# Kernel optimization log

Hardware: AMD Instinct MI355X
Metric: run time of the kernel (lower is better)

The kernel has to match this reference:

```python
import jax, jax.numpy as jnp
import numpy as np
from jax import lax

D_MAX = 6.4; GRID_RES = 0.1; G = 9.81; MASS = 40.0
K_STIFF = 5000.0; K_DAMP = float(np.sqrt(4.0 * MASS * K_STIFF)); K_FRIC = 0.5
DT = 0.01; N_STEPS = 500; EPS = 1e-6


def _robot_geometry():
    # DPhysConfig.rigid_body_geometry(from_mesh=False), robot_size=(1.0, 0.5)
    xs = np.concatenate([np.linspace(-0.5, 0.5, 8), np.linspace(-0.5, 0.5, 8)])
    ys = np.concatenate([0.25 * np.ones(8), -0.25 * np.ones(8)])
    zz = np.array([0.2, 0.1, 0.0, 0.0, 0.0, 0.0, 0.1, 0.2])
    zs = np.concatenate([zz, zz])
    pts = np.stack([xs, ys, zs], 1).astype(np.float32)
    cog = pts.mean(0)
    return pts, (pts[:, 1] > cog[1]), (pts[:, 1] < cog[1])


def _inertia_inv(mass, pts):
    n = pts.shape[0]; mp = mass / n
    x, y, z = pts[:, 0], pts[:, 1], pts[:, 2]
    Ixx = (mp * (y**2 + z**2)).sum(); Iyy = (mp * (x**2 + z**2)).sum(); Izz = (mp * (x**2 + y**2)).sum()
    Ixy = -(mp * x * y).sum(); Ixz = -(mp * x * z).sum(); Iyz = -(mp * y * z).sum()
    I = np.array([[Ixx, Ixy, Ixz], [Ixy, Iyy, Iyz], [Ixz, Iyz, Izz]], dtype=np.float64) * 10.0
    return np.linalg.inv(I).astype(np.float32)


def _interp(grid, xq, yq):
    # bilinear interpolation of (B,H,W) grid at metric query points (B,N)
    B, H, W = grid.shape
    xi = jnp.clip((xq + D_MAX) / GRID_RES, 0.0, H - 2)
    yi = jnp.clip((yq + D_MAX) / GRID_RES, 0.0, W - 2)
    x0 = jnp.floor(xi).astype(jnp.int32); y0 = jnp.floor(yi).astype(jnp.int32)
    b = jnp.arange(B)[:, None]
    z00 = grid[b, x0, y0];     z10 = grid[b, x0 + 1, y0]
    z01 = grid[b, x0, y0 + 1]; z11 = grid[b, x0 + 1, y0 + 1]
    wx = xi - x0; wy = yi - y0
    return z00 * (1 - wx) * (1 - wy) + z10 * wx * (1 - wy) + z01 * (1 - wx) * wy + z11 * wx * wy


def _normals(grid, xq, yq):
    e = GRID_RES
    dzdx = (_interp(grid, xq + e, yq) - _interp(grid, xq - e, yq)) / (2 * e)
    dzdy = (_interp(grid, xq, yq + e) - _interp(grid, xq, yq - e)) / (2 * e)
    n = jnp.stack([-dzdx, -dzdy, jnp.ones_like(dzdx)], -1)
    return n / (jnp.linalg.norm(n, axis=-1, keepdims=True) + EPS)


def _skew(v):
    z = jnp.zeros_like(v[..., 0])
    return jnp.stack([
        jnp.stack([z, -v[..., 2], v[..., 1]], -1),
        jnp.stack([v[..., 2], z, -v[..., 0]], -1),
        jnp.stack([-v[..., 1], v[..., 0], z], -1)], -2)


def _rk4(x, xd, dt):
    k1 = dt * xd
    k2 = dt * (xd + k1 / 2)
    k3 = dt * (xd + k2 / 2)
    k4 = dt * (xd + k3)
    return x + (k1 + 2 * k2 + 2 * k3 + k4) / 6


def _integrate_rotation(R, omega, dt):
    Ox = _skew(omega)                                  # (B,3,3)
    theta = jnp.linalg.norm(omega, axis=-1)[:, None, None]
    Oxn = Ox / (theta + EPS)
    I3 = jnp.eye(3, dtype=R.dtype)
    return R @ (I3 + Oxn * jnp.sin(theta * dt) + (Oxn @ Oxn) * (1 - jnp.cos(theta * dt)))


def _forward_sim(z_grid, controls, robot_points, I_inv, mask_left, mask_right):
    B = z_grid.shape[0]; n_pts = robot_points.shape[0]
    dt = jnp.float32(DT)
    x = jnp.zeros((B, 3), z_grid.dtype).at[:, 2].set(1.0)
    xd = jnp.zeros((B, 3), z_grid.dtype)
    R = jnp.broadcast_to(jnp.eye(3, dtype=z_grid.dtype), (B, 3, 3))
    omega = jnp.zeros((B, 3), z_grid.dtype)
    x_points = x[:, None, :] + robot_points[None]      # (B,n,3)
    xd_points = jnp.zeros((B, n_pts, 3), z_grid.dtype)
    ml = mask_left[None, :, None]; mr = mask_right[None, :, None]

    def step(carry, u):
        x, xd, R, omega, x_points, xd_points = carry
        u_left, u_right = u[:, 0], u[:, 1]
        # --- forward_kinematics ---
        z_pts = _interp(z_grid, x_points[..., 0], x_points[..., 1])[..., None]
        dh = x_points[..., 2:3] - z_pts
        on_grid = ((x_points[..., 0:1] >= -D_MAX) & (x_points[..., 0:1] <= D_MAX) &
                   (x_points[..., 1:2] >= -D_MAX) & (x_points[..., 1:2] <= D_MAX))
        in_contact = ((dh <= 0.0) & on_grid).astype(x_points.dtype)
        n = _normals(z_grid, x_points[..., 0], x_points[..., 1])   # (B,n,3)
        xd_n = (xd_points * n).sum(-1, keepdims=True)
        F_spring = -(K_STIFF * dh + K_DAMP * xd_n) * n * in_contact
        thrust = R[..., 0]                                         # R @ [1,0,0]
        thrust = thrust / (jnp.linalg.norm(thrust, axis=-1, keepdims=True) + EPS)
        N = jnp.linalg.norm(F_spring, axis=2)[..., None]           # (B,n,1)
        v_l = (u_left[:, None] * thrust)[:, None, :]
        v_r = (u_right[:, None] * thrust)[:, None, :]
        f_l = K_FRIC * N * jnp.tanh(v_l - xd_points)
        f_r = K_FRIC * N * jnp.tanh(v_r - xd_points)
        F_fric = jnp.where(ml, f_l, jnp.where(mr, f_r, jnp.zeros_like(f_l)))
        r = x_points - x[:, None, :]
        torque = jnp.cross(r, F_spring + F_fric).sum(1)            # (B,3)
        omega_d = torque @ I_inv.T
        F_cog = jnp.array([0.0, 0.0, -MASS * G], z_grid.dtype) + F_spring.mean(1) + F_fric.mean(1)
        xdd = F_cog / MASS
        xd_pts_new = xd[:, None, :] + jnp.cross(omega[:, None, :], r)
        # --- update_state ---
        xd_new = _rk4(xd, xdd, dt)
        x_new = _rk4(x, xd_new, dt)
        x_points_new = _rk4(x_points, xd_pts_new, dt)
        omega_new = _rk4(omega, omega_d, dt)
        R_new = _integrate_rotation(R, omega_new, dt)
        carry_new = (x_new, xd_new, R_new, omega_new, x_points_new, xd_pts_new)
        out = jnp.concatenate([x_new, xd_new, omega_new, R_new.reshape(B, 9),
                               x_points_new.reshape(B, -1),
                               F_spring.reshape(B, -1), F_fric.reshape(B, -1)], -1)
        return carry_new, out

    _, traj = lax.scan(step, (x, xd, R, omega, x_points, xd_points),
                       jnp.swapaxes(controls, 0, 1))
    return jnp.swapaxes(traj, 0, 1)   # (B, T, 3+3+3+9+48+48+48=162)


def setup_inputs() -> dict:
    key = jax.random.key(0)
    k1, k2 = jax.random.split(key)
    B, H, W, T = 256, 128, 128, N_STEPS
    pts, ml, mr = _robot_geometry()
    z_grid = 0.1 * jax.random.normal(k1, (B, H, W), dtype=jnp.float32)
    controls = jax.random.uniform(k2, (B, T, 2), dtype=jnp.float32, minval=-1.2, maxval=1.2)
    return {
        "z_grid": z_grid,
        "controls": controls,
        "robot_points": jnp.asarray(pts),
        "I_inv": jnp.asarray(_inertia_inv(MASS, pts)),
        "mask_left": jnp.asarray(ml),
        "mask_right": jnp.asarray(mr),
    }


def reference(z_grid, controls, robot_points, I_inv, mask_left, mask_right):
    return _forward_sim(z_grid, controls, robot_points, I_inv, mask_left, mask_right)
```

## Files before the change

### kernel.cpp

```cpp
#include <hip/hip_runtime.h>
#include <math.h>

#define HGRID 128
#define WGRID 128
#define NPTS 16
#define TSTEPS 500

__device__ __forceinline__ float dpp_sum16(float v) {
    int x;
    x = __builtin_amdgcn_update_dpp(0, __float_as_int(v), 0xB1, 0xF, 0xF, true);
    v += __int_as_float(x);
    x = __builtin_amdgcn_update_dpp(0, __float_as_int(v), 0x4E, 0xF, 0xF, true);
    v += __int_as_float(x);
    x = __builtin_amdgcn_update_dpp(0, __float_as_int(v), 0x141, 0xF, 0xF, true);
    v += __int_as_float(x);
    x = __builtin_amdgcn_update_dpp(0, __float_as_int(v), 0x140, 0xF, 0xF, true);
    v += __int_as_float(x);
    return v;
}

__device__ __forceinline__ float interp1(const float* __restrict__ sg, float xq, float yq) {
    float xi = (xq + 6.4f) / 0.1f;
    xi = fminf(fmaxf(xi, 0.0f), 126.0f);
    float yi = (yq + 6.4f) / 0.1f;
    yi = fminf(fmaxf(yi, 0.0f), 126.0f);
    float fx = floorf(xi);
    float fy = floorf(yi);
    int x0 = (int)fx;
    int y0 = (int)fy;
    float wx = xi - fx;
    float wy = yi - fy;
    const float* r0 = sg + (x0 * WGRID + y0);
    float z00 = r0[0];
    float z01 = r0[1];
    float z10 = r0[WGRID];
    float z11 = r0[WGRID + 1];
    float ox = 1.0f - wx, oy = 1.0f - wy;
    return z00 * ox * oy + z10 * wx * oy + z01 * ox * wy + z11 * wx * wy;
}

extern "C" __global__ __launch_bounds__(64, 1) void dphys_sim(
    const float* __restrict__ z_grid,
    const float* __restrict__ controls,
    const float* __restrict__ robot_points,
    const float* __restrict__ I_inv,
    float* __restrict__ out)
{
    __shared__ float sg[HGRID * WGRID];

    const int b = blockIdx.x;
    const int lane = threadIdx.x;

    {
        const float4* src = (const float4*)(z_grid + (size_t)b * (HGRID * WGRID));
        float4* dst = (float4*)sg;
        #pragma unroll 4
        for (int i = lane; i < (HGRID * WGRID) / 4; i += 64) dst[i] = src[i];
    }

    const float i00 = I_inv[0], i01 = I_inv[1], i02 = I_inv[2];
    const float i10 = I_inv[3], i11 = I_inv[4], i12 = I_inv[5];
    const float i20 = I_inv[6], i21 = I_inv[7], i22 = I_inv[8];

    const int p = lane & 15;
    const float rpx = robot_points[3 * p + 0];
    const float rpy = robot_points[3 * p + 1];
    const float rpz = robot_points[3 * p + 2];

    const float cog_y = dpp_sum16(rpy) * (1.0f / 16.0f);
    const bool is_left = rpy > cog_y;

    __syncthreads();

    const float K_STIFF = 5000.0f;
    const float K_DAMP  = 894.4271909999159f;
    const float K_FRIC  = 0.5f;
    const float DTC     = 0.01f;
    const float EPSF    = 1e-6f;
    const float CRK     = 0.010050166708416667f;

    float X = 0.f, Y = 0.f, Z = 1.f;
    float VX = 0.f, VY = 0.f, VZ = 0.f;
    float R00 = 1.f, R01 = 0.f, R02 = 0.f;
    float R10 = 0.f, R11 = 1.f, R12 = 0.f;
    float R20 = 0.f, R21 = 0.f, R22 = 1.f;
    float OX = 0.f, OY = 0.f, OZ = 0.f;
    float px = rpx, py = rpy, pz = rpz + 1.0f;
    float pvx = 0.f, pvy = 0.f, pvz = 0.f;

    float* outb = out + (size_t)b * TSTEPS * 162;
    const float* cg = controls + (size_t)b * (TSTEPS * 2);

    float u_l = cg[0], u_r = cg[1];

    #pragma unroll 1
    for (int t = 0; t < TSTEPS; ++t) {
        const int tn = (t + 1 < TSTEPS) ? (t + 1) : t;
        const float u_l_nxt = cg[2 * tn + 0];
        const float u_r_nxt = cg[2 * tn + 1];

        const float z_pt = interp1(sg, px, py);
        const float zpx  = interp1(sg, px + 0.1f, py);
        const float zmx  = interp1(sg, px - 0.1f, py);
        const float zpy  = interp1(sg, px, py + 0.1f);
        const float zmy  = interp1(sg, px, py - 0.1f);

        const float dh = pz - z_pt;
        const bool on = (px >= -6.4f) && (px <= 6.4f) && (py >= -6.4f) && (py <= 6.4f);
        const float contact = ((dh <= 0.0f) && on) ? 1.0f : 0.0f;

        const float dzdx = (zpx - zmx) / 0.2f;
        const float dzdy = (zpy - zmy) / 0.2f;
        float nx = -dzdx, ny = -dzdy, nz = 1.0f;
        const float nn = sqrtf(nx * nx + ny * ny + nz * nz) + EPSF;
        nx /= nn; ny /= nn; nz /= nn;

        const float xd_n = pvx * nx + pvy * ny + pvz * nz;
        const float s_mag = -(K_STIFF * dh + K_DAMP * xd_n);
        const float fsx = s_mag * nx * contact;
        const float fsy = s_mag * ny * contact;
        const float fsz = s_mag * nz * contact;

        const float Nmag = sqrtf(fsx * fsx + fsy * fsy + fsz * fsz);

        float tx = R00, ty = R10, tz = R20;
        const float tnn = sqrtf(tx * tx + ty * ty + tz * tz) + EPSF;
        tx /= tnn; ty /= tnn; tz /= tnn;

        const float u_sel = is_left ? u_l : u_r;
        const float kn = K_FRIC * Nmag;
        const float ffx = kn * tanhf(u_sel * tx - pvx);
        const float ffy = kn * tanhf(u_sel * ty - pvy);
        const float ffz = kn * tanhf(u_sel * tz - pvz);

        const float rx = px - X, ry = py - Y, rz = pz - Z;
        const float Fx = fsx + ffx, Fy = fsy + ffy, Fz = fsz + ffz;
        const float tqx = ry * Fz - rz * Fy;
        const float tqy = rz * Fx - rx * Fz;
        const float tqz = rx * Fy - ry * Fx;

        const float Tqx = dpp_sum16(tqx);
        const float Tqy = dpp_sum16(tqy);
        const float Tqz = dpp_sum16(tqz);
        const float Ssx = dpp_sum16(fsx);
        const float Ssy = dpp_sum16(fsy);
        const float Ssz = dpp_sum16(fsz);
        const float Sfx = dpp_sum16(ffx);
        const float Sfy = dpp_sum16(ffy);
        const float Sfz = dpp_sum16(ffz);

        const float odx = i00 * Tqx + i01 * Tqy + i02 * Tqz;
        const float ody = i10 * Tqx + i11 * Tqy + i12 * Tqz;
        const float odz = i20 * Tqx + i21 * Tqy + i22 * Tqz;

        const float Fcx = Ssx * 0.0625f + Sfx * 0.0625f;
        const float Fcy = Ssy * 0.0625f + Sfy * 0.0625f;
        const float Fcz = -392.4f + Ssz * 0.0625f + Sfz * 0.0625f;
        const float axd = Fcx / 40.0f;
        const float ayd = Fcy / 40.0f;
        const float azd = Fcz / 40.0f;

        const float cpx = OY * rz - OZ * ry;
        const float cpy = OZ * rx - OX * rz;
        const float cpz = OX * ry - OY * rx;
        const float pvnx = VX + cpx, pvny = VY + cpy, pvnz = VZ + cpz;

        const float VXn = fmaf(axd, CRK, VX);
        const float VYn = fmaf(ayd, CRK, VY);
        const float VZn = fmaf(azd, CRK, VZ);
        const float Xn = fmaf(VXn, CRK, X);
        const float Yn = fmaf(VYn, CRK, Y);
        const float Zn = fmaf(VZn, CRK, Z);
        const float pxn = fmaf(pvnx, CRK, px);
        const float pyn = fmaf(pvny, CRK, py);
        const float pzn = fmaf(pvnz, CRK, pz);
        const float OXn = fmaf(odx, CRK, OX);
        const float OYn = fmaf(ody, CRK, OY);
        const float OZn = fmaf(odz, CRK, OZ);

        const float th = sqrtf(OXn * OXn + OYn * OYn + OZn * OZn);
        const float inv = 1.0f / (th + EPSF);
        const float axn = OXn * inv, ayn = OYn * inv, azn = OZn * inv;
        const float sth = sinf(th * DTC);
        const float cth = 1.0f - cosf(th * DTC);
        const float M00 = 1.0f - (ayn * ayn + azn * azn) * cth;
        const float M01 = -azn * sth + axn * ayn * cth;
        const float M02 =  ayn * sth + axn * azn * cth;
        const float M10 =  azn * sth + axn * ayn * cth;
        const float M11 = 1.0f - (axn * axn + azn * azn) * cth;
        const float M12 = -axn * sth + ayn * azn * cth;
        const float M20 = -ayn * sth + axn * azn * cth;
        const float M21 =  axn * sth + ayn * azn * cth;
        const float M22 = 1.0f - (axn * axn + ayn * ayn) * cth;

        const float nR00 = R00 * M00 + R01 * M10 + R02 * M20;
        const float nR01 = R00 * M01 + R01 * M11 + R02 * M21;
        const float nR02 = R00 * M02 + R01 * M12 + R02 * M22;
        const float nR10 = R10 * M00 + R11 * M10 + R12 * M20;
        const float nR11 = R10 * M01 + R11 * M11 + R12 * M21;
        const float nR12 = R10 * M02 + R11 * M12 + R12 * M22;
        const float nR20 = R20 * M00 + R21 * M10 + R22 * M20;
        const float nR21 = R20 * M01 + R21 * M11 + R22 * M21;
        const float nR22 = R20 * M02 + R21 * M12 + R22 * M22;

        float* ob = outb + (size_t)t * 162;
        if (lane == 0) {
            ob[0] = Xn;  ob[1] = Yn;  ob[2] = Zn;
            ob[3] = VXn; ob[4] = VYn; ob[5] = VZn;
            ob[6] = OXn; ob[7] = OYn; ob[8] = OZn;
            ob[9]  = nR00; ob[10] = nR01; ob[11] = nR02;
            ob[12] = nR10; ob[13] = nR11; ob[14] = nR12;
            ob[15] = nR20; ob[16] = nR21; ob[17] = nR22;
        }
        if (lane < 16) {
            float* o1 = ob + 18 + 3 * lane;
            o1[0] = pxn; o1[1] = pyn; o1[2] = pzn;
            float* o2 = ob + 66 + 3 * lane;
            o2[0] = fsx; o2[1] = fsy; o2[2] = fsz;
            float* o3 = ob + 114 + 3 * lane;
            o3[0] = ffx; o3[1] = ffy; o3[2] = ffz;
        }

        X = Xn; Y = Yn; Z = Zn;
        VX = VXn; VY = VYn; VZ = VZn;
        px = pxn; py = pyn; pz = pzn;
        pvx = pvnx; pvy = pvny; pvz = pvnz;
        OX = OXn; OY = OYn; OZ = OZn;
        R00 = nR00; R01 = nR01; R02 = nR02;
        R10 = nR10; R11 = nR11; R12 = nR12;
        R20 = nR20; R21 = nR21; R22 = nR22;

        u_l = u_l_nxt; u_r = u_r_nxt;
    }
}

extern "C" void kernel_launch(void* const* d_in, const int* in_sizes, int n_in,
                              void* d_out, int out_size, void* d_ws, size_t ws_size,
                              hipStream_t stream) {
    const float* z_grid       = (const float*)d_in[0];
    const float* controls     = (const float*)d_in[1];
    const float* robot_points = (const float*)d_in[2];
    const float* I_inv        = (const float*)d_in[3];
    float* out = (float*)d_out;

    const int B = in_sizes[0] / (HGRID * WGRID);
    dphys_sim<<<dim3(B), dim3(64), 0, stream>>>(z_grid, controls, robot_points, I_inv, out);
}
```

Baseline: 902.0 us.

## Read height grid from global memory and prefetch next step's interpolation taps

Drops the shared-memory copy of the 64KB height grid and reads bilinear taps straight from global memory (L1/L2). To hide that latency, the next step's point positions are computed at the top of the loop so the 20 grid loads for step t+1 are issued before step t's force computation. This gives up LDS latency in exchange for global-cache latency, which the overlap is meant to hide, and removes the upfront grid copy and the barrier. It also adds register pressure to carry 30 prefetched values across the loop.

```diff
diff --git a/kernel.cpp b/kernel.cpp
--- a/kernel.cpp
+++ b/kernel.cpp
@@ -1,9 +1,8 @@
 #include <hip/hip_runtime.h>
 #include <math.h>
 
+#define WGRID 128
 #define HGRID 128
-#define WGRID 128
-#define NPTS 16
 #define TSTEPS 500
 
 __device__ __forceinline__ float dpp_sum16(float v) {
@@ -19,24 +18,28 @@
     return v;
 }
 
-__device__ __forceinline__ float interp1(const float* __restrict__ sg, float xq, float yq) {
-    float xi = (xq + 6.4f) / 0.1f;
+struct Ax { int i0; float w; };
+__device__ __forceinline__ Ax axq(float q) {
+    float xi = (q + 6.4f) / 0.1f;
     xi = fminf(fmaxf(xi, 0.0f), 126.0f);
-    float yi = (yq + 6.4f) / 0.1f;
-    yi = fminf(fmaxf(yi, 0.0f), 126.0f);
-    float fx = floorf(xi);
-    float fy = floorf(yi);
-    int x0 = (int)fx;
-    int y0 = (int)fy;
-    float wx = xi - fx;
-    float wy = yi - fy;
-    const float* r0 = sg + (x0 * WGRID + y0);
-    float z00 = r0[0];
-    float z01 = r0[1];
-    float z10 = r0[WGRID];
-    float z11 = r0[WGRID + 1];
-    float ox = 1.0f - wx, oy = 1.0f - wy;
-    return z00 * ox * oy + z10 * wx * oy + z01 * ox * wy + z11 * wx * wy;
+    float f = floorf(xi);
+    Ax a; a.i0 = (int)f; a.w = xi - f; return a;
+}
+
+struct Iq { float z00, z01, z10, z11, wx, wy; };
+__device__ __forceinline__ Iq issueQ(const float* __restrict__ zb, Ax ax, Ax ay) {
+    const float* r0 = zb + (ax.i0 * WGRID + ay.i0);
+    Iq q;
+    q.z00 = r0[0];
+    q.z01 = r0[1];
+    q.z10 = r0[WGRID];
+    q.z11 = r0[WGRID + 1];
+    q.wx = ax.w; q.wy = ay.w;
+    return q;
+}
+__device__ __forceinline__ float combineQ(Iq q) {
+    float ox = 1.0f - q.wx, oy = 1.0f - q.wy;
+    return q.z00 * ox * oy + q.z10 * q.wx * oy + q.z01 * ox * q.wy + q.z11 * q.wx * q.wy;
 }
 
 extern "C" __global__ __launch_bounds__(64, 1) void dphys_sim(
@@ -46,17 +49,10 @@
     const float* __restrict__ I_inv,
     float* __restrict__ out)
 {
-    __shared__ float sg[HGRID * WGRID];
-
     const int b = blockIdx.x;
     const int lane = threadIdx.x;
 
-    {
-        const float4* src = (const float4*)(z_grid + (size_t)b * (HGRID * WGRID));
-        float4* dst = (float4*)sg;
-        #pragma unroll 4
-        for (int i = lane; i < (HGRID * WGRID) / 4; i += 64) dst[i] = src[i];
-    }
+    const float* __restrict__ zb = z_grid + (size_t)b * (HGRID * WGRID);
 
     const float i00 = I_inv[0], i01 = I_inv[1], i02 = I_inv[2];
     const float i10 = I_inv[3], i11 = I_inv[4], i12 = I_inv[5];
@@ -70,12 +66,9 @@
     const float cog_y = dpp_sum16(rpy) * (1.0f / 16.0f);
     const bool is_left = rpy > cog_y;
 
-    __syncthreads();
-
     const float K_STIFF = 5000.0f;
     const float K_DAMP  = 894.4271909999159f;
     const float K_FRIC  = 0.5f;
-    const float DTC     = 0.01f;
     const float EPSF    = 1e-6f;
     const float CRK     = 0.010050166708416667f;
 
@@ -93,17 +86,41 @@
 
     float u_l = cg[0], u_r = cg[1];
 
+    Ax ax0 = axq(px), axp = axq(px + 0.1f), axm = axq(px - 0.1f);
+    Ax ay0 = axq(py), ayp = axq(py + 0.1f), aym = axq(py - 0.1f);
+    Iq qc  = issueQ(zb, ax0, ay0);
+    Iq qxp = issueQ(zb, axp, ay0);
+    Iq qxm = issueQ(zb, axm, ay0);
+    Iq qyp = issueQ(zb, ax0, ayp);
+    Iq qym = issueQ(zb, ax0, aym);
+
     #pragma unroll 1
     for (int t = 0; t < TSTEPS; ++t) {
         const int tn = (t + 1 < TSTEPS) ? (t + 1) : t;
         const float u_l_nxt = cg[2 * tn + 0];
         const float u_r_nxt = cg[2 * tn + 1];
 
-        const float z_pt = interp1(sg, px, py);
-        const float zpx  = interp1(sg, px + 0.1f, py);
-        const float zmx  = interp1(sg, px - 0.1f, py);
-        const float zpy  = interp1(sg, px, py + 0.1f);
-        const float zmy  = interp1(sg, px, py - 0.1f);
+        const float rx = px - X, ry = py - Y, rz = pz - Z;
+        const float pvnx = VX + (OY * rz - OZ * ry);
+        const float pvny = VY + (OZ * rx - OX * rz);
+        const float pvnz = VZ + (OX * ry - OY * rx);
+        const float pxn = fmaf(pvnx, CRK, px);
+        const float pyn = fmaf(pvny, CRK, py);
+        const float pzn = fmaf(pvnz, CRK, pz);
+
+        Ax nax0 = axq(pxn), naxp = axq(pxn + 0.1f), naxm = axq(pxn - 0.1f);
+        Ax nay0 = axq(pyn), nayp = axq(pyn + 0.1f), naym = axq(pyn - 0.1f);
+        Iq nqc  = issueQ(zb, nax0, nay0);
+        Iq nqxp = issueQ(zb, naxp, nay0);
+        Iq nqxm = issueQ(zb, naxm, nay0);
+        Iq nqyp = issueQ(zb, nax0, nayp);
+        Iq nqym = issueQ(zb, nax0, naym);
+
+        const float z_pt = combineQ(qc);
+        const float zpx  = combineQ(qxp);
+        const float zmx  = combineQ(qxm);
+        const float zpy  = combineQ(qyp);
+        const float zmy  = combineQ(qym);
 
         const float dh = pz - z_pt;
         const bool on = (px >= -6.4f) && (px <= 6.4f) && (py >= -6.4f) && (py <= 6.4f);
@@ -133,7 +150,6 @@
         const float ffy = kn * tanhf(u_sel * ty - pvy);
         const float ffz = kn * tanhf(u_sel * tz - pvz);
 
-        const float rx = px - X, ry = py - Y, rz = pz - Z;
         const float Fx = fsx + ffx, Fy = fsy + ffy, Fz = fsz + ffz;
         const float tqx = ry * Fz - rz * Fy;
         const float tqy = rz * Fx - rx * Fz;
@@ -160,29 +176,22 @@
         const float ayd = Fcy / 40.0f;
         const float azd = Fcz / 40.0f;
 
-        const float cpx = OY * rz - OZ * ry;
-        const float cpy = OZ * rx - OX * rz;
-        const float cpz = OX * ry - OY * rx;
-        const float pvnx = VX + cpx, pvny = VY + cpy, pvnz = VZ + cpz;
-
         const float VXn = fmaf(axd, CRK, VX);
         const float VYn = fmaf(ayd, CRK, VY);
         const float VZn = fmaf(azd, CRK, VZ);
         const float Xn = fmaf(VXn, CRK, X);
         const float Yn = fmaf(VYn, CRK, Y);
         const float Zn = fmaf(VZn, CRK, Z);
-        const float pxn = fmaf(pvnx, CRK, px);
-        const float pyn = fmaf(pvny, CRK, py);
-        const float pzn = fmaf(pvnz, CRK, pz);
         const float OXn = fmaf(odx, CRK, OX);
         const float OYn = fmaf(ody, CRK, OY);
         const float OZn = fmaf(odz, CRK, OZ);
 
         const float th = sqrtf(OXn * OXn + OYn * OYn + OZn * OZn);
-        const float inv = 1.0f / (th + EPSF);
-        const float axn = OXn * inv, ayn = OYn * inv, azn = OZn * inv;
-        const float sth = sinf(th * DTC);
-        const float cth = 1.0f - cosf(th * DTC);
+        const float tpe = th + EPSF;
+        const float axn = OXn / tpe, ayn = OYn / tpe, azn = OZn / tpe;
+        const float ang = th * 0.01f;
+        const float sth = sinf(ang);
+        const float cth = 1.0f - cosf(ang);
         const float M00 = 1.0f - (ayn * ayn + azn * azn) * cth;
         const float M01 = -azn * sth + axn * ayn * cth;
         const float M02 =  ayn * sth + axn * azn * cth;
@@ -229,7 +238,7 @@
         R00 = nR00; R01 = nR01; R02 = nR02;
         R10 = nR10; R11 = nR11; R12 = nR12;
         R20 = nR20; R21 = nR21; R22 = nR22;
-
+        qc = nqc; qxp = nqxp; qxm = nqxm; qyp = nqyp; qym = nqym;
         u_l = u_l_nxt; u_r = u_r_nxt;
     }
 }
```

Result: slower. 920.5 us (+2.0%).

## Swizzle shared-memory grid layout and share axis interpolation terms

Applied to the files above, without the earlier changes.

Grid rows are stored in LDS with an XOR swizzle on the column index so that the 16 points gathering nearby rows hit fewer conflicting banks. The per-axis floor and weight math is computed once per offset and reused across the five bilinear lookups. The time loop is now unrolled by 2, and the axis normalisation uses divisions instead of multiplying by a reciprocal. The swizzle adds integer ops to every load, and the unroll may raise register pressure.

```diff
diff --git a/kernel.cpp b/kernel.cpp
--- a/kernel.cpp
+++ b/kernel.cpp
@@ -1,9 +1,8 @@
 #include <hip/hip_runtime.h>
 #include <math.h>
 
+#define WGRID 128
 #define HGRID 128
-#define WGRID 128
-#define NPTS 16
 #define TSTEPS 500
 
 __device__ __forceinline__ float dpp_sum16(float v) {
@@ -19,23 +18,24 @@
     return v;
 }
 
-__device__ __forceinline__ float interp1(const float* __restrict__ sg, float xq, float yq) {
-    float xi = (xq + 6.4f) / 0.1f;
+struct Ax { int i0; float w; };
+__device__ __forceinline__ Ax axq(float q) {
+    float xi = (q + 6.4f) / 0.1f;
     xi = fminf(fmaxf(xi, 0.0f), 126.0f);
-    float yi = (yq + 6.4f) / 0.1f;
-    yi = fminf(fmaxf(yi, 0.0f), 126.0f);
-    float fx = floorf(xi);
-    float fy = floorf(yi);
-    int x0 = (int)fx;
-    int y0 = (int)fy;
-    float wx = xi - fx;
-    float wy = yi - fy;
-    const float* r0 = sg + (x0 * WGRID + y0);
-    float z00 = r0[0];
-    float z01 = r0[1];
-    float z10 = r0[WGRID];
-    float z11 = r0[WGRID + 1];
-    float ox = 1.0f - wx, oy = 1.0f - wy;
+    float f = floorf(xi);
+    Ax a; a.i0 = (int)f; a.w = xi - f; return a;
+}
+
+__device__ __forceinline__ float ldsQ(const float* __restrict__ sg, Ax ax, Ax ay) {
+    const int r0 = ax.i0, c0 = ay.i0;
+    const int m0 = r0 & 28;
+    const int m1 = (r0 + 1) & 28;
+    const float z00 = sg[(r0 << 7) + (c0 ^ m0)];
+    const float z01 = sg[(r0 << 7) + ((c0 + 1) ^ m0)];
+    const float z10 = sg[((r0 + 1) << 7) + (c0 ^ m1)];
+    const float z11 = sg[((r0 + 1) << 7) + ((c0 + 1) ^ m1)];
+    const float wx = ax.w, wy = ay.w;
+    const float ox = 1.0f - wx, oy = 1.0f - wy;
     return z00 * ox * oy + z10 * wx * oy + z01 * ox * wy + z11 * wx * wy;
 }
 
@@ -53,9 +53,14 @@
 
     {
         const float4* src = (const float4*)(z_grid + (size_t)b * (HGRID * WGRID));
-        float4* dst = (float4*)sg;
         #pragma unroll 4
-        for (int i = lane; i < (HGRID * WGRID) / 4; i += 64) dst[i] = src[i];
+        for (int i = lane; i < (HGRID * WGRID) / 4; i += 64) {
+            const float4 v = src[i];
+            const int row = i >> 5;
+            const int colblk = (i & 31) << 2;
+            const int scol = colblk ^ (row & 28);
+            *(float4*)&sg[(row << 7) + scol] = v;
+        }
     }
 
     const float i00 = I_inv[0], i01 = I_inv[1], i02 = I_inv[2];
@@ -75,7 +80,6 @@
     const float K_STIFF = 5000.0f;
     const float K_DAMP  = 894.4271909999159f;
     const float K_FRIC  = 0.5f;
-    const float DTC     = 0.01f;
     const float EPSF    = 1e-6f;
     const float CRK     = 0.010050166708416667f;
 
@@ -93,17 +97,19 @@
 
     float u_l = cg[0], u_r = cg[1];
 
-    #pragma unroll 1
+    #pragma unroll 2
     for (int t = 0; t < TSTEPS; ++t) {
         const int tn = (t + 1 < TSTEPS) ? (t + 1) : t;
         const float u_l_nxt = cg[2 * tn + 0];
         const float u_r_nxt = cg[2 * tn + 1];
 
-        const float z_pt = interp1(sg, px, py);
-        const float zpx  = interp1(sg, px + 0.1f, py);
-        const float zmx  = interp1(sg, px - 0.1f, py);
-        const float zpy  = interp1(sg, px, py + 0.1f);
-        const float zmy  = interp1(sg, px, py - 0.1f);
+        Ax ax0 = axq(px), axp = axq(px + 0.1f), axm = axq(px - 0.1f);
+        Ax ay0 = axq(py), ayp = axq(py + 0.1f), aym = axq(py - 0.1f);
+        const float z_pt = ldsQ(sg, ax0, ay0);
+        const float zpx  = ldsQ(sg, axp, ay0);
+        const float zmx  = ldsQ(sg, axm, ay0);
+        const float zpy  = ldsQ(sg, ax0, ayp);
+        const float zmy  = ldsQ(sg, ax0, aym);
 
         const float dh = pz - z_pt;
         const bool on = (px >= -6.4f) && (px <= 6.4f) && (py >= -6.4f) && (py <= 6.4f);
@@ -179,10 +185,11 @@
         const float OZn = fmaf(odz, CRK, OZ);
 
         const float th = sqrtf(OXn * OXn + OYn * OYn + OZn * OZn);
-        const float inv = 1.0f / (th + EPSF);
-        const float axn = OXn * inv, ayn = OYn * inv, azn = OZn * inv;
-        const float sth = sinf(th * DTC);
-        const float cth = 1.0f - cosf(th * DTC);
+        const float tpe = th + EPSF;
+        const float axn = OXn / tpe, ayn = OYn / tpe, azn = OZn / tpe;
+        const float ang = th * 0.01f;
+        const float sth = sinf(ang);
+        const float cth = 1.0f - cosf(ang);
         const float M00 = 1.0f - (ayn * ayn + azn * azn) * cth;
         const float M01 = -azn * sth + axn * ayn * cth;
         const float M02 =  ayn * sth + axn * azn * cth;
@@ -229,7 +236,6 @@
         R00 = nR00; R01 = nR01; R02 = nR02;
         R10 = nR10; R11 = nR11; R12 = nR12;
         R20 = nR20; R21 = nR21; R22 = nR22;
-
         u_l = u_l_nxt; u_r = u_r_nxt;
     }
 }
```

Result: no change. 898.0 us (-0.4%).
